# Optimization experiments

Measured on AMD Instinct MI355X. Metric: run time of the kernel, lower is better.

The kernel has to match this reference:

```python
import jax, jax.numpy as jnp
import numpy as np

B, N, IN_F, OUT_F, H = 4, 1024, 256, 256, 8
HID = OUT_F // H  # 32
ALPHA = 0.2  # leaky relu negative slope


def setup_inputs() -> dict:
    key = jax.random.key(0)
    k1, k2, k3, k4 = jax.random.split(key, 4)
    h = jax.random.normal(k1, (B, N, IN_F), dtype=jnp.float32)
    # linear: in_features -> n_heads*n_hidden, no bias (stored as [in, out])
    W = jax.random.normal(k2, (IN_F, H * HID), dtype=jnp.float32) / np.sqrt(IN_F)
    # attn: Linear(2*n_hidden, 1, bias=False), shared across heads
    attn_w = jax.random.normal(k3, (2 * HID,), dtype=jnp.float32) / np.sqrt(2 * HID)
    # random dense adjacency (p=0.5) plus self loops, broadcast over heads
    u = jax.random.uniform(k4, (B, N, N, 1), dtype=jnp.float32)
    adj_mat = jnp.maximum((u < 0.5).astype(jnp.float32), jnp.eye(N, dtype=jnp.float32)[None, :, :, None])
    return {"h": h, "adj_mat": adj_mat, "W": W, "attn_w": attn_w}


def reference(h, adj_mat, W, attn_w):
    # g: [b, n, h, d]
    g = (h @ W).reshape(B, N, H, HID)
    # attn(concat(g_i, g_j)) decomposes: e[b,i,j,h] = <attn_w[:HID], g_i> + <attn_w[HID:], g_j>
    # (exactly the math of the repeat/repeat_interleave/cat + 1-wide linear, without the N^2 concat)
    e_i = jnp.einsum('bnhd,d->bnh', g, attn_w[:HID])   # g_repeat_interleave part (index i)
    e_j = jnp.einsum('bnhd,d->bnh', g, attn_w[HID:])   # g_repeat part (index j)
    e = e_i[:, :, None, :] + e_j[:, None, :, :]        # [b, i, j, h]
    e = jnp.where(e >= 0, e, ALPHA * e)                # LeakyReLU(alpha)
    e = jnp.where(adj_mat == 0, -jnp.inf, e)           # masked_fill
    a = jax.nn.softmax(e, axis=1)                      # faithful: original uses Softmax(dim=1)
    # dropout p acts as identity in eval mode / p=0
    out = jnp.einsum('bijh,bjhd->bihd', a, g)          # [b, i, h, d]
    return out.reshape(B, N, H * HID)                  # is_concat=True
```

## Files before the change

### kernel.cpp

```cpp
#include <hip/hip_runtime.h>
#include <math.h>

#define BB 4
#define NN 1024
#define HH 8
#define NROW (BB*NN)

typedef short s8v __attribute__((ext_vector_type(8)));
typedef float f4v __attribute__((ext_vector_type(4)));

__device__ __forceinline__ float lrelu(float x) { return fmaxf(x, 0.2f * x); }
__device__ __forceinline__ short bf16rne(float f) {
    unsigned u = __float_as_uint(f);
    u += 0x7FFF + ((u >> 16) & 1u);
    return (short)(u >> 16);
}

__global__ __launch_bounds__(256) void k_gemm_ei(const float* __restrict__ hm,
                                                 const float* __restrict__ W,
                                                 const float* __restrict__ aw,
                                                 float* __restrict__ g,
                                                 float* __restrict__ e_i,
                                                 float* __restrict__ e_j,
                                                 float* __restrict__ e_jt) {
    __shared__ __align__(16) float hs[8][256];
    __shared__ float aws[64];
    const int row0 = blockIdx.x * 8;
    const int t = threadIdx.x;
    if (t < 64) aws[t] = aw[t];
    const float4* h4 = (const float4*)(hm + row0 * 256);
    float4* hs4 = (float4*)&hs[0][0];
    hs4[t] = h4[t];
    hs4[t + 256] = h4[t + 256];
    __syncthreads();

    float c0 = 0.f, c1 = 0.f, c2 = 0.f, c3 = 0.f, c4 = 0.f, c5 = 0.f, c6 = 0.f, c7 = 0.f;
    for (int k4 = 0; k4 < 64; ++k4) {
        const float w0 = W[(4 * k4 + 0) * 256 + t];
        const float w1 = W[(4 * k4 + 1) * 256 + t];
        const float w2 = W[(4 * k4 + 2) * 256 + t];
        const float w3 = W[(4 * k4 + 3) * 256 + t];
#define ROW(r)                                                        \
        {                                                             \
            const float4 hv = *(const float4*)&hs[r][4 * k4];         \
            c##r = fmaf(hv.x, w0, c##r);                              \
            c##r = fmaf(hv.y, w1, c##r);                              \
            c##r = fmaf(hv.z, w2, c##r);                              \
            c##r = fmaf(hv.w, w3, c##r);                              \
        }
        ROW(0) ROW(1) ROW(2) ROW(3) ROW(4) ROW(5) ROW(6) ROW(7)
#undef ROW
    }
    const int d = t & 31, hh = t >> 5;
    const int b = row0 >> 10;
#define EPI(r)                                                                  \
    {                                                                           \
        g[(row0 + r) * 256 + t] = c##r;                                         \
        float vi = c##r * aws[d];                                               \
        float vj = c##r * aws[32 + d];                                          \
        for (int mm = 1; mm < 32; mm <<= 1) {                                   \
            vi += __shfl_xor(vi, mm);                                           \
            vj += __shfl_xor(vj, mm);                                           \
        }                                                                       \
        if (d == 0) {                                                           \
            e_i[(row0 + r) * 8 + hh] = vi;                                      \
            e_j[(row0 + r) * 8 + hh] = vj;                                      \
            e_jt[(size_t)(b * 8 + hh) * NN + ((row0 + r) & (NN - 1))] = vj;     \
        }                                                                       \
    }
    EPI(0) EPI(1) EPI(2) EPI(3) EPI(4) EPI(5) EPI(6) EPI(7)
#undef EPI
}

__global__ __launch_bounds__(256) void k_s(const float* __restrict__ adj,
                                           const float* __restrict__ e_i,
                                           const float* __restrict__ e_j,
                                           float* __restrict__ ps) {
    __shared__ __align__(16) float eis[128 * 8];
    __shared__ float ejs[8][64];
    __shared__ float sp[4][8][64];
    const int bx = blockIdx.x;
    const int b = bx >> 7, jc = (bx >> 3) & 15, ic = bx & 7;
    const int j0 = jc * 64, i0 = ic * 128;
    const int t = threadIdx.x;

    ((float4*)eis)[t] = ((const float4*)(e_i + (b * NN + i0) * 8))[t];
    if (t < 128) {
        const float4 v = ((const float4*)(e_j + (b * NN + j0) * 8))[t];
        const int base = t * 4;
        ejs[(base + 0) & 7][(base + 0) >> 3] = v.x;
        ejs[(base + 1) & 7][(base + 1) >> 3] = v.y;
        ejs[(base + 2) & 7][(base + 2) >> 3] = v.z;
        ejs[(base + 3) & 7][(base + 3) >> 3] = v.w;
    }
    __syncthreads();

    const int ii = t >> 6, jj = t & 63;
    const float e0 = ejs[0][jj], e1 = ejs[1][jj], e2 = ejs[2][jj], e3 = ejs[3][jj];
    const float e4 = ejs[4][jj], e5 = ejs[5][jj], e6 = ejs[6][jj], e7 = ejs[7][jj];
    float s0 = 0.f, s1 = 0.f, s2 = 0.f, s3 = 0.f, s4 = 0.f, s5 = 0.f, s6 = 0.f, s7 = 0.f;
    const float* adjp = adj + (size_t)b * NN * NN + j0 + jj;
    for (int i = ii; i < 128; i += 4) {
        const float a = adjp[(size_t)(i0 + i) * NN];
        const f4v eA = *(const f4v*)&eis[i * 8];
        const f4v eB = *(const f4v*)&eis[i * 8 + 4];
        s0 = fmaf(a, __expf(lrelu(eA[0] + e0)), s0);
        s1 = fmaf(a, __expf(lrelu(eA[1] + e1)), s1);
        s2 = fmaf(a, __expf(lrelu(eA[2] + e2)), s2);
        s3 = fmaf(a, __expf(lrelu(eA[3] + e3)), s3);
        s4 = fmaf(a, __expf(lrelu(eB[0] + e4)), s4);
        s5 = fmaf(a, __expf(lrelu(eB[1] + e5)), s5);
        s6 = fmaf(a, __expf(lrelu(eB[2] + e6)), s6);
        s7 = fmaf(a, __expf(lrelu(eB[3] + e7)), s7);
    }
    sp[ii][0][jj] = s0; sp[ii][1][jj] = s1; sp[ii][2][jj] = s2; sp[ii][3][jj] = s3;
    sp[ii][4][jj] = s4; sp[ii][5][jj] = s5; sp[ii][6][jj] = s6; sp[ii][7][jj] = s7;
    __syncthreads();
#pragma unroll
    for (int k = 0; k < 2; ++k) {
        const int idx = t * 2 + k;
        const int jjo = idx >> 3, h = idx & 7;
        const float s = sp[0][h][jjo] + sp[1][h][jjo] + sp[2][h][jjo] + sp[3][h][jjo];
        ps[ic * (NROW * 8) + (b * NN + j0 + jjo) * 8 + h] = s;
    }
}

__global__ __launch_bounds__(256) void k_prep(const float* __restrict__ ps,
                                              const float* __restrict__ g,
                                              short* __restrict__ Gt) {
    __shared__ float rss[16][8];
    const int bx = blockIdx.x;
    const int b = bx >> 6, j0 = (bx & 63) * 16;
    const int t = threadIdx.x;
    if (t < 128) {
        const int jj = t >> 3, h = t & 7;
        float s = 0.f;
#pragma unroll
        for (int ic = 0; ic < 8; ++ic)
            s += ps[ic * (NROW * 8) + (b * NN + j0 + jj) * 8 + h];
        rss[jj][h] = 1.0f / s;
    }
    __syncthreads();
    const int h = t >> 5, d = t & 31;
    uint4 w0, w1;
#define PK(dst, r0, r1)                                                          \
    {                                                                            \
        const float va = g[(size_t)(b * NN + j0 + r0) * 256 + t] * rss[r0][h];   \
        const float vb = g[(size_t)(b * NN + j0 + r1) * 256 + t] * rss[r1][h];   \
        dst = (unsigned)(unsigned short)bf16rne(va) |                            \
              ((unsigned)(unsigned short)bf16rne(vb) << 16);                     \
    }
    PK(w0.x, 0, 1) PK(w0.y, 2, 3) PK(w0.z, 4, 5) PK(w0.w, 6, 7)
    PK(w1.x, 8, 9) PK(w1.y, 10, 11) PK(w1.z, 12, 13) PK(w1.w, 14, 15)
#undef PK
    const int jt = j0 >> 5, jj0 = j0 & 31;
    short* dst = Gt + ((size_t)((b * 8 + h) * 32 + jt)) * 1024 + d * 32 + jj0;
    *(uint4*)dst = w0;
    *(uint4*)(dst + 8) = w1;
}

__global__ __launch_bounds__(256) void k_out_mfma(const float* __restrict__ adj,
                                                  const short* __restrict__ Gt,
                                                  const float* __restrict__ e_i,
                                                  const float* __restrict__ e_jt,
                                                  float* __restrict__ out) {
    __shared__ short gts[4][4][32][40];
    __shared__ float ejt[4][128];
    const int bx = blockIdx.x;
    const int hs = bx >> 8, b = (bx >> 6) & 3, i0 = (bx & 63) * 16;
    const int t = threadIdx.x;
    const int wave = t >> 6, lane = t & 63;
    const int m = lane & 15, q = lane >> 4;
    const int h = hs * 4 + wave;

    const float ei = e_i[(size_t)(b * NN + i0 + m) * 8 + h];
    f4v acc0 = {0.f, 0.f, 0.f, 0.f}, acc1 = {0.f, 0.f, 0.f, 0.f};

    const float* adjrow = adj + (size_t)b * NN * NN + (size_t)(i0 + m) * NN;
    const float4* gtg4 = (const float4*)Gt;
    const float4* ejt4 = (const float4*)(e_jt + (size_t)b * 8 * NN);

#define LGD(k, sv, dst)                                                          \
    {                                                                            \
        const int u = t + 256 * (k);                                             \
        dst = gtg4[(size_t)(b * 8 + hs * 4 + (u >> 9)) * 4096 + (sv) * 512 +     \
                   (u & 511)];                                                   \
    }
#define LAD(sv, lt, half, dst)                                                   \
    dst = *(const f4v*)&adjrow[(sv) * 128 + (lt) * 32 + q * 8 + (half) * 4];

    float4 g0, g1, g2, g3, g4, g5, g6, g7;
    f4v a0, a1, a2, a3, a4, a5, a6, a7;
    float4 ev = make_float4(0.f, 0.f, 0.f, 0.f);
    LGD(0, 0, g0) LGD(1, 0, g1) LGD(2, 0, g2) LGD(3, 0, g3)
    LGD(4, 0, g4) LGD(5, 0, g5) LGD(6, 0, g6) LGD(7, 0, g7)
    LAD(0, 0, 0, a0) LAD(0, 0, 1, a1) LAD(0, 1, 0, a2) LAD(0, 1, 1, a3)
    LAD(0, 2, 0, a4) LAD(0, 2, 1, a5) LAD(0, 3, 0, a6) LAD(0, 3, 1, a7)
    if (t < 128) ev = ejt4[(size_t)(hs * 4 + (t >> 5)) * 256 + (t & 31)];

    for (int s = 0; s < 8; ++s) {
        __syncthreads();
#define SG(k, src)                                                               \
        {                                                                        \
            const int u = t + 256 * (k);                                         \
            char* dstp = (char*)gts + (u >> 9) * 10240 + ((u >> 7) & 3) * 2560 + \
                         ((u >> 2) & 31) * 80 + (u & 3) * 16;                    \
            *(float4*)dstp = src;                                                \
        }
        SG(0, g0) SG(1, g1) SG(2, g2) SG(3, g3)
        SG(4, g4) SG(5, g5) SG(6, g6) SG(7, g7)
#undef SG
        if (t < 128) *(float4*)&ejt[t >> 5][(t & 31) * 4] = ev;
        __syncthreads();

        const int sn = (s + 1) & 7;
        float4 ng0, ng1, ng2, ng3, ng4, ng5, ng6, ng7;
        f4v na0, na1, na2, na3, na4, na5, na6, na7;
        float4 nev = make_float4(0.f, 0.f, 0.f, 0.f);
        LGD(0, sn, ng0) LGD(1, sn, ng1) LGD(2, sn, ng2) LGD(3, sn, ng3)
        LGD(4, sn, ng4) LGD(5, sn, ng5) LGD(6, sn, ng6) LGD(7, sn, ng7)
        LAD(sn, 0, 0, na0) LAD(sn, 0, 1, na1) LAD(sn, 1, 0, na2) LAD(sn, 1, 1, na3)
        LAD(sn, 2, 0, na4) LAD(sn, 2, 1, na5) LAD(sn, 3, 0, na6) LAD(sn, 3, 1, na7)
        if (t < 128) nev = ejt4[(size_t)(hs * 4 + (t >> 5)) * 256 + sn * 32 + (t & 31)];

#define LT(lt, aA, aB)                                                            \
        {                                                                         \
            const f4v ej0 = *(const f4v*)&ejt[wave][(lt) * 32 + q * 8];           \
            const f4v ej1 = *(const f4v*)&ejt[wave][(lt) * 32 + q * 8 + 4];       \
            s8v A;                                                                \
            A[0] = bf16rne(aA[0] * __expf(lrelu(ei + ej0[0])));                   \
            A[1] = bf16rne(aA[1] * __expf(lrelu(ei + ej0[1])));                   \
            A[2] = bf16rne(aA[2] * __expf(lrelu(ei + ej0[2])));                   \
            A[3] = bf16rne(aA[3] * __expf(lrelu(ei + ej0[3])));                   \
            A[4] = bf16rne(aB[0] * __expf(lrelu(ei + ej1[0])));                   \
            A[5] = bf16rne(aB[1] * __expf(lrelu(ei + ej1[1])));                   \
            A[6] = bf16rne(aB[2] * __expf(lrelu(ei + ej1[2])));                   \
            A[7] = bf16rne(aB[3] * __expf(lrelu(ei + ej1[3])));                   \
            const s8v B0 = *(const s8v*)&gts[wave][lt][m][q * 8];                 \
            const s8v B1 = *(const s8v*)&gts[wave][lt][m + 16][q * 8];            \
            acc0 = __builtin_amdgcn_mfma_f32_16x16x32_bf16(A, B0, acc0, 0, 0, 0); \
            acc1 = __builtin_amdgcn_mfma_f32_16x16x32_bf16(A, B1, acc1, 0, 0, 0); \
        }
        LT(0, a0, a1) LT(1, a2, a3) LT(2, a4, a5) LT(3, a6, a7)
#undef LT

        g0 = ng0; g1 = ng1; g2 = ng2; g3 = ng3;
        g4 = ng4; g5 = ng5; g6 = ng6; g7 = ng7;
        a0 = na0; a1 = na1; a2 = na2; a3 = na3;
        a4 = na4; a5 = na5; a6 = na6; a7 = na7;
        ev = nev;
    }
#undef LGD
#undef LAD

    float* op = out + (size_t)(b * NN + i0) * 256;
#pragma unroll
    for (int r = 0; r < 4; ++r) {
        const int row = q * 4 + r;
        op[(size_t)row * 256 + h * 32 + m] = acc0[r];
        op[(size_t)row * 256 + h * 32 + 16 + m] = acc1[r];
    }
}

extern "C" void kernel_launch(void* const* d_in, const int* in_sizes, int n_in,
                              void* d_out, int out_size, void* d_ws, size_t ws_size,
                              hipStream_t stream) {
    const float* h      = (const float*)d_in[0];
    const float* adj    = (const float*)d_in[1];
    const float* W      = (const float*)d_in[2];
    const float* attn_w = (const float*)d_in[3];
    float* out = (float*)d_out;

    float* ws = (float*)d_ws;
    float* g    = ws;
    float* e_i  = g + NROW * 256;
    float* e_j  = e_i + NROW * 8;
    float* e_jt = e_j + NROW * 8;
    float* ps   = e_jt + NROW * 8;
    short* Gt   = (short*)(ps + 8 * NROW * 8);

    k_gemm_ei<<<NROW / 8, 256, 0, stream>>>(h, W, attn_w, g, e_i, e_j, e_jt);
    k_s<<<512, 256, 0, stream>>>(adj, e_i, e_j, ps);
    k_prep<<<256, 256, 0, stream>>>(ps, g, Gt);
    k_out_mfma<<<512, 256, 0, stream>>>(adj, Gt, e_i, e_jt, out);
}
```

Before: 127.0 us.

## Pack adjacency into bitmask in k_s and read bits in output kernel

k_s now ballots the nonzero adjacency entries into 64-bit masks per row chunk and writes them to workspace. The output MFMA kernel reads these compact bits instead of re-reading the full fp32 adjacency matrix, removing a large second pass over the adjacency. The register double-buffered prefetch of the next stage was dropped at the same time, so global loads are now issued within each stage, which may expose more latency.

```diff
diff --git a/kernel.cpp b/kernel.cpp
--- a/kernel.cpp
+++ b/kernel.cpp
@@ -75,7 +75,8 @@
 __global__ __launch_bounds__(256) void k_s(const float* __restrict__ adj,
                                            const float* __restrict__ e_i,
                                            const float* __restrict__ e_j,
-                                           float* __restrict__ ps) {
+                                           float* __restrict__ ps,
+                                           unsigned long long* __restrict__ bits) {
     __shared__ __align__(16) float eis[128 * 8];
     __shared__ float ejs[8][64];
     __shared__ float sp[4][8][64];
@@ -102,6 +103,8 @@
     const float* adjp = adj + (size_t)b * NN * NN + j0 + jj;
     for (int i = ii; i < 128; i += 4) {
         const float a = adjp[(size_t)(i0 + i) * NN];
+        const unsigned long long mk = __ballot(a != 0.f);
+        if (jj == 0) bits[(size_t)(b * NN + i0 + i) * 16 + jc] = mk;
         const f4v eA = *(const f4v*)&eis[i * 8];
         const f4v eB = *(const f4v*)&eis[i * 8 + 4];
         s0 = fmaf(a, __expf(lrelu(eA[0] + e0)), s0);
@@ -159,7 +162,7 @@
     *(uint4*)(dst + 8) = w1;
 }
 
-__global__ __launch_bounds__(256) void k_out_mfma(const float* __restrict__ adj,
+__global__ __launch_bounds__(256) void k_out_mfma(const unsigned long long* __restrict__ bits,
                                                   const short* __restrict__ Gt,
                                                   const float* __restrict__ e_i,
                                                   const float* __restrict__ e_jt,
@@ -176,82 +179,60 @@
     const float ei = e_i[(size_t)(b * NN + i0 + m) * 8 + h];
     f4v acc0 = {0.f, 0.f, 0.f, 0.f}, acc1 = {0.f, 0.f, 0.f, 0.f};
 
-    const float* adjrow = adj + (size_t)b * NN * NN + (size_t)(i0 + m) * NN;
+    const unsigned long long* bitsrow = bits + (size_t)(b * NN + i0 + m) * 16;
     const float4* gtg4 = (const float4*)Gt;
     const float4* ejt4 = (const float4*)(e_jt + (size_t)b * 8 * NN);
 
-#define LGD(k, sv, dst)                                                          \
-    {                                                                            \
-        const int u = t + 256 * (k);                                             \
-        dst = gtg4[(size_t)(b * 8 + hs * 4 + (u >> 9)) * 4096 + (sv) * 512 +     \
-                   (u & 511)];                                                   \
-    }
-#define LAD(sv, lt, half, dst)                                                   \
-    dst = *(const f4v*)&adjrow[(sv) * 128 + (lt) * 32 + q * 8 + (half) * 4];
-
-    float4 g0, g1, g2, g3, g4, g5, g6, g7;
-    f4v a0, a1, a2, a3, a4, a5, a6, a7;
-    float4 ev = make_float4(0.f, 0.f, 0.f, 0.f);
-    LGD(0, 0, g0) LGD(1, 0, g1) LGD(2, 0, g2) LGD(3, 0, g3)
-    LGD(4, 0, g4) LGD(5, 0, g5) LGD(6, 0, g6) LGD(7, 0, g7)
-    LAD(0, 0, 0, a0) LAD(0, 0, 1, a1) LAD(0, 1, 0, a2) LAD(0, 1, 1, a3)
-    LAD(0, 2, 0, a4) LAD(0, 2, 1, a5) LAD(0, 3, 0, a6) LAD(0, 3, 1, a7)
-    if (t < 128) ev = ejt4[(size_t)(hs * 4 + (t >> 5)) * 256 + (t & 31)];
-
     for (int s = 0; s < 8; ++s) {
+        float4 g0, g1, g2, g3, g4, g5, g6, g7;
+#define LG(k)                                                                     \
+        {                                                                         \
+            const int u = t + 256 * (k);                                          \
+            g##k = gtg4[(size_t)(b * 8 + hs * 4 + (u >> 9)) * 4096 + s * 512 +    \
+                        (u & 511)];                                               \
+        }
+        LG(0) LG(1) LG(2) LG(3) LG(4) LG(5) LG(6) LG(7)
+#undef LG
+        const ulonglong2 bv = *(const ulonglong2*)&bitsrow[s * 2];
+        float4 ev = make_float4(0.f, 0.f, 0.f, 0.f);
+        if (t < 128) ev = ejt4[(size_t)(hs * 4 + (t >> 5)) * 256 + s * 32 + (t & 31)];
         __syncthreads();
-#define SG(k, src)                                                               \
-        {                                                                        \
-            const int u = t + 256 * (k);                                         \
-            char* dstp = (char*)gts + (u >> 9) * 10240 + ((u >> 7) & 3) * 2560 + \
-                         ((u >> 2) & 31) * 80 + (u & 3) * 16;                    \
-            *(float4*)dstp = src;                                                \
-        }
-        SG(0, g0) SG(1, g1) SG(2, g2) SG(3, g3)
-        SG(4, g4) SG(5, g5) SG(6, g6) SG(7, g7)
+#define SG(k)                                                                     \
+        {                                                                         \
+            const int u = t + 256 * (k);                                          \
+            char* dstp = (char*)gts + (u >> 9) * 10240 + ((u >> 7) & 3) * 2560 +  \
+                         ((u >> 2) & 31) * 80 + (u & 3) * 16;                     \
+            *(float4*)dstp = g##k;                                                \
+        }
+        SG(0) SG(1) SG(2) SG(3) SG(4) SG(5) SG(6) SG(7)
 #undef SG
         if (t < 128) *(float4*)&ejt[t >> 5][(t & 31) * 4] = ev;
         __syncthreads();
 
-        const int sn = (s + 1) & 7;
-        float4 ng0, ng1, ng2, ng3, ng4, ng5, ng6, ng7;
-        f4v na0, na1, na2, na3, na4, na5, na6, na7;
-        float4 nev = make_float4(0.f, 0.f, 0.f, 0.f);
-        LGD(0, sn, ng0) LGD(1, sn, ng1) LGD(2, sn, ng2) LGD(3, sn, ng3)
-        LGD(4, sn, ng4) LGD(5, sn, ng5) LGD(6, sn, ng6) LGD(7, sn, ng7)
-        LAD(sn, 0, 0, na0) LAD(sn, 0, 1, na1) LAD(sn, 1, 0, na2) LAD(sn, 1, 1, na3)
-        LAD(sn, 2, 0, na4) LAD(sn, 2, 1, na5) LAD(sn, 3, 0, na6) LAD(sn, 3, 1, na7)
-        if (t < 128) nev = ejt4[(size_t)(hs * 4 + (t >> 5)) * 256 + sn * 32 + (t & 31)];
-
-#define LT(lt, aA, aB)                                                            \
+        const unsigned bw0 = (unsigned)bv.x, bw1 = (unsigned)(bv.x >> 32);
+        const unsigned bw2 = (unsigned)bv.y, bw3 = (unsigned)(bv.y >> 32);
+
+#define LT(lt, bw)                                                                \
         {                                                                         \
             const f4v ej0 = *(const f4v*)&ejt[wave][(lt) * 32 + q * 8];           \
             const f4v ej1 = *(const f4v*)&ejt[wave][(lt) * 32 + q * 8 + 4];       \
             s8v A;                                                                \
-            A[0] = bf16rne(aA[0] * __expf(lrelu(ei + ej0[0])));                   \
-            A[1] = bf16rne(aA[1] * __expf(lrelu(ei + ej0[1])));                   \
-            A[2] = bf16rne(aA[2] * __expf(lrelu(ei + ej0[2])));                   \
-            A[3] = bf16rne(aA[3] * __expf(lrelu(ei + ej0[3])));                   \
-            A[4] = bf16rne(aB[0] * __expf(lrelu(ei + ej1[0])));                   \
-            A[5] = bf16rne(aB[1] * __expf(lrelu(ei + ej1[1])));                   \
-            A[6] = bf16rne(aB[2] * __expf(lrelu(ei + ej1[2])));                   \
-            A[7] = bf16rne(aB[3] * __expf(lrelu(ei + ej1[3])));                   \
+            A[0] = ((bw >> (q * 8 + 0)) & 1u) ? bf16rne(__expf(lrelu(ei + ej0[0]))) : (short)0; \
+            A[1] = ((bw >> (q * 8 + 1)) & 1u) ? bf16rne(__expf(lrelu(ei + ej0[1]))) : (short)0; \
+            A[2] = ((bw >> (q * 8 + 2)) & 1u) ? bf16rne(__expf(lrelu(ei + ej0[2]))) : (short)0; \
+            A[3] = ((bw >> (q * 8 + 3)) & 1u) ? bf16rne(__expf(lrelu(ei + ej0[3]))) : (short)0; \
+            A[4] = ((bw >> (q * 8 + 4)) & 1u) ? bf16rne(__expf(lrelu(ei + ej1[0]))) : (short)0; \
+            A[5] = ((bw >> (q * 8 + 5)) & 1u) ? bf16rne(__expf(lrelu(ei + ej1[1]))) : (short)0; \
+            A[6] = ((bw >> (q * 8 + 6)) & 1u) ? bf16rne(__expf(lrelu(ei + ej1[2]))) : (short)0; \
+            A[7] = ((bw >> (q * 8 + 7)) & 1u) ? bf16rne(__expf(lrelu(ei + ej1[3]))) : (short)0; \
             const s8v B0 = *(const s8v*)&gts[wave][lt][m][q * 8];                 \
             const s8v B1 = *(const s8v*)&gts[wave][lt][m + 16][q * 8];            \
             acc0 = __builtin_amdgcn_mfma_f32_16x16x32_bf16(A, B0, acc0, 0, 0, 0); \
             acc1 = __builtin_amdgcn_mfma_f32_16x16x32_bf16(A, B1, acc1, 0, 0, 0); \
         }
-        LT(0, a0, a1) LT(1, a2, a3) LT(2, a4, a5) LT(3, a6, a7)
+        LT(0, bw0) LT(1, bw1) LT(2, bw2) LT(3, bw3)
 #undef LT
-
-        g0 = ng0; g1 = ng1; g2 = ng2; g3 = ng3;
-        g4 = ng4; g5 = ng5; g6 = ng6; g7 = ng7;
-        a0 = na0; a1 = na1; a2 = na2; a3 = na3;
-        a4 = na4; a5 = na5; a6 = na6; a7 = na7;
-        ev = nev;
-    }
-#undef LGD
-#undef LAD
+    }
 
     float* op = out + (size_t)(b * NN + i0) * 256;
 #pragma unroll
@@ -278,9 +259,10 @@
     float* e_jt = e_j + NROW * 8;
     float* ps   = e_jt + NROW * 8;
     short* Gt   = (short*)(ps + 8 * NROW * 8);
+    unsigned long long* bits = (unsigned long long*)(Gt + 2 * 1048576);
 
     k_gemm_ei<<<NROW / 8, 256, 0, stream>>>(h, W, attn_w, g, e_i, e_j, e_jt);
-    k_s<<<512, 256, 0, stream>>>(adj, e_i, e_j, ps);
+    k_s<<<512, 256, 0, stream>>>(adj, e_i, e_j, ps, bits);
     k_prep<<<256, 256, 0, stream>>>(ps, g, Gt);
-    k_out_mfma<<<512, 256, 0, stream>>>(adj, Gt, e_i, e_jt, out);
-}
+    k_out_mfma<<<512, 256, 0, stream>>>(bits, Gt, e_i, e_jt, out);
+}
```

New measurement: 129.2 us. No clear change (+1.7%).
